# Kernel tuning notes

Hardware: AMD Instinct MI355X
Metric: run time of the kernel (lower is better)

Reference implementation:

```python
import jax, jax.numpy as jnp
import numpy as np

P_DROP = 0.6  # F.dropout default training=True in the original forward

def setup_inputs() -> dict:
    key = jax.random.key(0)
    k1, k2, k3, k4 = jax.random.split(key, 4)
    B, T, V, F, K, O = 32, 12, 1000, 64, 3, 64
    x = jax.random.normal(k1, (B, T, V, F), dtype=jnp.float32)
    Att = jax.random.uniform(k2, (V, V), dtype=jnp.float32)
    cheb = jax.random.normal(k3, (K, V, V), dtype=jnp.float32)   # Chebyshev polynomials T_k(L)
    Theta = jax.random.normal(k4, (K, F, O), dtype=jnp.float32)  # per-order feature transforms
    return {"x": x, "Att": Att, "cheb": cheb, "Theta": Theta}

def reference(x, Att, cheb, Theta):
    # x: [B,T,V,F]; Att: [V,V]; cheb: [K,V,V]; Theta: [K,F,O]
    B, T, V, F = x.shape
    K = cheb.shape[0]
    keep = 1.0 - P_DROP
    # Original draws a fresh dropout mask per (time_step, k); replicate with a fixed key.
    mask = jax.random.bernoulli(jax.random.key(42), keep, (T, K, V, V))
    TkA = cheb * Att                                   # [K,V,V] attention-weighted polynomial
    M = jnp.where(mask, TkA[None] / keep, 0.0)         # [T,K,V,V] inverted dropout
    # rhs = T_k_with_at @ graph_signal, batched over (b,t,k)
    rhs = jnp.einsum('tkuv,btvf->btkuf', M, x)         # [B,T,K,V,F]
    # sum_k rhs_k @ Theta_k  -> [B,T,V,O]; matches permute(0,3,1,2) of stacked outputs
    out = jnp.einsum('btkuf,kfo->btuo', rhs, Theta)
    return jax.nn.relu(out)
```

## Files before the change

kernel.cpp:

```cpp
#include <hip/hip_runtime.h>
#include <hip/hip_bf16.h>
#include <stdint.h>


typedef __attribute__((ext_vector_type(8))) short short8;
typedef __attribute__((ext_vector_type(4))) float f32x4;

__device__ __forceinline__ ushort f2bf(float f) {
  __hip_bfloat16 h = __float2bfloat16(f);
  return *reinterpret_cast<ushort*>(&h);
}

__device__ __forceinline__ void threefry2x32(uint32_t c0, uint32_t c1,
                                             uint32_t& o0, uint32_t& o1) {
  const uint32_t ks0 = 0u;
  const uint32_t ks1 = 42u;
  const uint32_t ks2 = ks0 ^ ks1 ^ 0x1BD11BDAu;
  uint32_t x0 = c0 + ks0;
  uint32_t x1 = c1 + ks1;
#define TFR(r) { x0 += x1; x1 = (x1 << (r)) | (x1 >> (32 - (r))); x1 ^= x0; }
  TFR(13) TFR(15) TFR(26) TFR(6)
  x0 += ks1; x1 += ks2 + 1u;
  TFR(17) TFR(29) TFR(16) TFR(24)
  x0 += ks2; x1 += ks0 + 2u;
  TFR(13) TFR(15) TFR(26) TFR(6)
  x0 += ks0; x1 += ks1 + 3u;
  TFR(17) TFR(29) TFR(16) TFR(24)
  x0 += ks1; x1 += ks2 + 4u;
  TFR(13) TFR(15) TFR(26) TFR(6)
  x0 += ks2; x1 += ks0 + 5u;
#undef TFR
  o0 = x0; o1 = x1;
}

__global__ void build_m(const float* __restrict__ Att,
                        const float* __restrict__ cheb,
                        ushort* __restrict__ Mws) {
  const uint32_t idx = blockIdx.x * 256u + threadIdx.x;
  const uint32_t vp = idx & 1023u;
  const uint32_t up = (idx >> 10) & 1023u;
  const uint32_t tk = idx >> 20;
  float val = 0.f;
  if ((vp < 1000u) & (up < 1000u)) {
    const uint32_t flat = (tk * 1000u + up) * 1000u + vp;
    uint32_t o0, o1;
    threefry2x32(0u, flat, o0, o1);
    const uint32_t bits = o0 ^ o1;
    const float u = __uint_as_float((bits >> 9) | 0x3f800000u) - 1.0f;
    if (u < 0.4f) {
      val = cheb[(tk % 3u) * 1000000u + up * 1000u + vp] *
            Att[up * 1000u + vp] * 2.5f;
    }
  }
  Mws[idx] = f2bf(val);
}

__global__ void transpose_x(const float* __restrict__ x,
                            ushort* __restrict__ xt) {
  __shared__ float lt[64][65];
  const int vc = blockIdx.x, t = blockIdx.y, b = blockIdx.z;
  const int tid = threadIdx.x;
  const int v0 = vc * 64;
#pragma unroll
  for (int i = 0; i < 4; ++i) {
    const int c = i * 256 + tid;
    const int vi = c >> 4, f4 = c & 15;
    float4 q = make_float4(0.f, 0.f, 0.f, 0.f);
    if (v0 + vi < 1000)
      q = *(const float4*)(x + ((((size_t)b * 12 + t) * 1000 + v0 + vi) << 6) + f4 * 4);
    lt[f4 * 4 + 0][vi] = q.x;
    lt[f4 * 4 + 1][vi] = q.y;
    lt[f4 * 4 + 2][vi] = q.z;
    lt[f4 * 4 + 3][vi] = q.w;
  }
  __syncthreads();
  const int f = tid >> 2, g = tid & 3;
  alignas(16) ushort tmp[16];
#pragma unroll
  for (int j = 0; j < 16; ++j) tmp[j] = f2bf(lt[f][g * 16 + j]);
  const size_t base = ((size_t)(t * 2048 + b * 64 + f)) << 10;
  *(uint4*)(xt + base + v0 + g * 16)     = *(const uint4*)&tmp[0];
  *(uint4*)(xt + base + v0 + g * 16 + 8) = *(const uint4*)&tmp[8];
}

#define LDT 72

#define MFMA(a, b, c) __builtin_amdgcn_mfma_f32_16x16x32_bf16((a), (b), (c), 0, 0, 0)

#define STAGE_LOAD(P0, P1, P2, P3, P4, P5, P6, P7, CO)                        \
  do {                                                                        \
    P0 = *(const uint4*)(Mws + ga0 + (CO));                                   \
    P1 = *(const uint4*)(Mws + ga1 + (CO));                                   \
    P2 = *(const uint4*)(Mws + ga0 + 1048576 + (CO));                         \
    P3 = *(const uint4*)(Mws + ga1 + 1048576 + (CO));                         \
    P4 = *(const uint4*)(Mws + ga0 + 2097152 + (CO));                         \
    P5 = *(const uint4*)(Mws + ga1 + 2097152 + (CO));                         \
    P6 = *(const uint4*)(xt + gx0 + (CO));                                    \
    P7 = *(const uint4*)(xt + gx1 + (CO));                                    \
  } while (0)

#define STAGE_WRITE(P0, P1, P2, P3, P4, P5, P6, P7, BP)                       \
  do {                                                                        \
    *(uint4*)&(BP)[da0]         = P0;                                         \
    *(uint4*)&(BP)[da1]         = P1;                                         \
    *(uint4*)&(BP)[8192 + da0]  = P2;                                         \
    *(uint4*)&(BP)[8192 + da1]  = P3;                                         \
    *(uint4*)&(BP)[16384 + da0] = P4;                                         \
    *(uint4*)&(BP)[16384 + da1] = P5;                                         \
    *(uint4*)&(BP)[24576 + da0] = P6;                                         \
    *(uint4*)&(BP)[24576 + da1] = P7;                                         \
  } while (0)

#define BURST(BP)                                                             \
  do {                                                                        \
    const ushort* sAc = (BP);                                                 \
    const ushort* sBc = (BP) + 24576;                                         \
    _Pragma("unroll")                                                         \
    for (int ks = 0; ks < 2; ++ks) {                                          \
      short8 bv[4];                                                           \
      _Pragma("unroll")                                                       \
      for (int ni = 0; ni < 4; ++ni) {                                        \
        const int row = wn * 64 + ni * 16 + l15;                              \
        bv[ni] = *(const short8*)&sBc[row * 64 + (((ks * 4 + quad) ^ rsw) * 8)]; \
      }                                                                       \
      _Pragma("unroll")                                                       \
      for (int k = 0; k < 3; ++k) {                                           \
        short8 av[2];                                                         \
        _Pragma("unroll")                                                     \
        for (int mi = 0; mi < 2; ++mi) {                                      \
          const int row = wu * 32 + mi * 16 + l15;                            \
          av[mi] = *(const short8*)&sAc[k * 8192 + row * 64 +                 \
                                        (((ks * 4 + quad) ^ rsw) * 8)];       \
        }                                                                     \
        _Pragma("unroll")                                                     \
        for (int mi = 0; mi < 2; ++mi)                                        \
          _Pragma("unroll")                                                   \
          for (int ni = 0; ni < 4; ++ni)                                      \
            pacc[k][mi][ni] = MFMA(av[mi], bv[ni], pacc[k][mi][ni]);          \
      }                                                                       \
    }                                                                         \
  } while (0)

#define SOFT_BARRIER()                                                        \
  do {                                                                        \
    asm volatile("s_waitcnt lgkmcnt(0)" ::: "memory");                        \
    __builtin_amdgcn_s_barrier();                                             \
    __builtin_amdgcn_sched_barrier(0);                                        \
  } while (0)

__global__ __launch_bounds__(512, 2)
void cheb_main(const ushort* __restrict__ Mws, const ushort* __restrict__ xt,
               const float* __restrict__ Theta, float* __restrict__ out) {
  __shared__ __align__(16) ushort smem[65536];
  const int tid = threadIdx.x;
  const int lane = tid & 63;
  const int w = tid >> 6;
  const int wu = w >> 1, wn = w & 1;
  const int quad = lane >> 4, l15 = lane & 15;
  const int nt = blockIdx.x, ut = blockIdx.y, t = blockIdx.z;
  const int u0 = ut * 128, n0 = nt * 128;

  ushort* buf0 = smem;
  ushort* buf1 = smem + 32768;
  ushort* sP  = smem + w * (32 * LDT);
  ushort* sTh = smem + 24576;

  const int srow = lane >> 3;
  const int gchunk = (lane & 7) ^ srow;
  const int rsw = l15 & 7;

  const size_t mbase = (size_t)(t * 3) << 20;
  const size_t xrow0 = (size_t)(t * 2048 + n0);

  const int rr0 = 8 * (w * 2 + 0) + srow;
  const int rr1 = 8 * (w * 2 + 1) + srow;
  const size_t ga0 = mbase + ((size_t)(u0 + rr0) << 10) + gchunk * 8;
  const size_t ga1 = mbase + ((size_t)(u0 + rr1) << 10) + gchunk * 8;
  const size_t gx0 = ((xrow0 + rr0) << 10) + gchunk * 8;
  const size_t gx1 = ((xrow0 + rr1) << 10) + gchunk * 8;
  const int da0 = (w * 2 + 0) * 512 + lane * 8;
  const int da1 = (w * 2 + 1) * 512 + lane * 8;

  f32x4 pacc[3][2][4];
#pragma unroll
  for (int k = 0; k < 3; ++k)
#pragma unroll
    for (int i = 0; i < 2; ++i)
#pragma unroll
      for (int j = 0; j < 4; ++j) pacc[k][i][j] = f32x4{0.f, 0.f, 0.f, 0.f};

  uint4 p0, p1, p2, p3, p4, p5, p6, p7;
  uint4 q0, q1, q2, q3, q4, q5, q6, q7;

  STAGE_LOAD(q0, q1, q2, q3, q4, q5, q6, q7, 0);
  STAGE_LOAD(p0, p1, p2, p3, p4, p5, p6, p7, 64);
  STAGE_WRITE(q0, q1, q2, q3, q4, q5, q6, q7, buf0);
  __syncthreads();

#pragma unroll 1
  for (int it = 0; it < 8; ++it) {
    const int vc = it * 2;
    if (vc < 14) STAGE_LOAD(q0, q1, q2, q3, q4, q5, q6, q7, (size_t)(vc + 2) * 64);
    __builtin_amdgcn_s_setprio(1);
    BURST(buf0);
    __builtin_amdgcn_s_setprio(0);
    if (vc < 15) STAGE_WRITE(p0, p1, p2, p3, p4, p5, p6, p7, buf1);
    SOFT_BARRIER();
    if (vc + 1 < 14) STAGE_LOAD(p0, p1, p2, p3, p4, p5, p6, p7, (size_t)(vc + 3) * 64);
    __builtin_amdgcn_s_setprio(1);
    BURST(buf1);
    __builtin_amdgcn_s_setprio(0);
    if (vc + 1 < 15) STAGE_WRITE(q0, q1, q2, q3, q4, q5, q6, q7, buf0);
    SOFT_BARRIER();
  }

  f32x4 oacc[2][4];
#pragma unroll
  for (int i = 0; i < 2; ++i)
#pragma unroll
    for (int j = 0; j < 4; ++j) oacc[i][j] = f32x4{0.f, 0.f, 0.f, 0.f};

#pragma unroll
  for (int k = 0; k < 3; ++k) {
    __syncthreads();
#pragma unroll
    for (int mi = 0; mi < 2; ++mi)
#pragma unroll
      for (int ni = 0; ni < 4; ++ni)
#pragma unroll
        for (int r = 0; r < 4; ++r)
          sP[(mi * 16 + quad * 4 + r) * LDT + ni * 16 + l15] = f2bf(pacc[k][mi][ni][r]);
    for (int e = tid; e < 4096; e += 512) {
      const int f = e >> 6, o = e & 63;
      sTh[o * LDT + f] = f2bf(Theta[k * 4096 + e]);
    }
    __syncthreads();
#pragma unroll
    for (int ks = 0; ks < 2; ++ks) {
      short8 a2[2], b2[4];
#pragma unroll
      for (int mi = 0; mi < 2; ++mi)
        a2[mi] = *(const short8*)&sP[(mi * 16 + l15) * LDT + ks * 32 + quad * 8];
#pragma unroll
      for (int ni = 0; ni < 4; ++ni)
        b2[ni] = *(const short8*)&sTh[(ni * 16 + l15) * LDT + ks * 32 + quad * 8];
#pragma unroll
      for (int mi = 0; mi < 2; ++mi)
#pragma unroll
        for (int ni = 0; ni < 4; ++ni)
          oacc[mi][ni] = MFMA(a2[mi], b2[ni], oacc[mi][ni]);
    }
  }

#pragma unroll
  for (int mi = 0; mi < 2; ++mi) {
    const int u_base = u0 + wu * 32 + mi * 16 + quad * 4;
#pragma unroll
    for (int ni = 0; ni < 4; ++ni) {
      const int n = n0 + wn * 64 + ni * 16 + l15;
      const int b = n >> 6, oo = n & 63;
      float* op = out + (((size_t)b * 12 + t) * 1000) * 64 + oo;
#pragma unroll
      for (int r = 0; r < 4; ++r) {
        const int u = u_base + r;
        if (u < 1000) op[(size_t)u * 64] = fmaxf(oacc[mi][ni][r], 0.f);
      }
    }
  }
}

extern "C" void kernel_launch(void* const* d_in, const int* in_sizes, int n_in,
                              void* d_out, int out_size, void* d_ws, size_t ws_size,
                              hipStream_t stream) {
  const float* x     = (const float*)d_in[0];
  const float* Att   = (const float*)d_in[1];
  const float* cheb  = (const float*)d_in[2];
  const float* Theta = (const float*)d_in[3];
  float* out = (float*)d_out;

  ushort* Mws = (ushort*)d_ws;
  ushort* xtw = Mws + 37748736ull;

  build_m<<<147456, 256, 0, stream>>>(Att, cheb, Mws);
  transpose_x<<<dim3(16, 12, 32), 256, 0, stream>>>(x, xtw);
  cheb_main<<<dim3(16, 8, 12), 512, 0, stream>>>(Mws, xtw, Theta, out);
}
```

Measured before the change: 295.3 us.

## Pre-swizzle M into MFMA fragment layout and load A operands directly to registers

build_m now writes the dropout-masked Chebyshev matrix in an MFMA-fragment-ordered layout, so cheb_main loads A operands straight from global memory into registers and no longer stages them through LDS. Only the x tile is double-buffered in shared memory, which shrinks the LDS footprint. The grid is flattened to 1D with ut as the fastest index, so blocks that share an x tile are adjacent. Launch bounds drop to one block per SM, and each lane now issues many uncoalesced-by-tile global loads per step, which risks exposed latency and more register pressure.

```diff
diff --git a/kernel.cpp b/kernel.cpp
--- a/kernel.cpp
+++ b/kernel.cpp
@@ -35,11 +35,16 @@
 
 __global__ void build_m(const float* __restrict__ Att,
                         const float* __restrict__ cheb,
-                        ushort* __restrict__ Mws) {
+                        ushort* __restrict__ Mf) {
   const uint32_t idx = blockIdx.x * 256u + threadIdx.x;
-  const uint32_t vp = idx & 1023u;
-  const uint32_t up = (idx >> 10) & 1023u;
+  const uint32_t j = idx & 7u;
+  const uint32_t lane = (idx >> 3) & 63u;
+  const uint32_t ks = (idx >> 9) & 1u;
+  const uint32_t c = (idx >> 10) & 15u;
+  const uint32_t u16 = (idx >> 14) & 63u;
   const uint32_t tk = idx >> 20;
+  const uint32_t up = u16 * 16u + (lane & 15u);
+  const uint32_t vp = c * 64u + ks * 32u + (lane >> 4) * 8u + j;
   float val = 0.f;
   if ((vp < 1000u) & (up < 1000u)) {
     const uint32_t flat = (tk * 1000u + up) * 1000u + vp;
@@ -52,7 +57,7 @@
             Att[up * 1000u + vp] * 2.5f;
     }
   }
-  Mws[idx] = f2bf(val);
+  Mf[idx] = f2bf(val);
 }
 
 __global__ void transpose_x(const float* __restrict__ x,
@@ -87,34 +92,9 @@
 
 #define MFMA(a, b, c) __builtin_amdgcn_mfma_f32_16x16x32_bf16((a), (b), (c), 0, 0, 0)
 
-#define STAGE_LOAD(P0, P1, P2, P3, P4, P5, P6, P7, CO)                        \
-  do {                                                                        \
-    P0 = *(const uint4*)(Mws + ga0 + (CO));                                   \
-    P1 = *(const uint4*)(Mws + ga1 + (CO));                                   \
-    P2 = *(const uint4*)(Mws + ga0 + 1048576 + (CO));                         \
-    P3 = *(const uint4*)(Mws + ga1 + 1048576 + (CO));                         \
-    P4 = *(const uint4*)(Mws + ga0 + 2097152 + (CO));                         \
-    P5 = *(const uint4*)(Mws + ga1 + 2097152 + (CO));                         \
-    P6 = *(const uint4*)(xt + gx0 + (CO));                                    \
-    P7 = *(const uint4*)(xt + gx1 + (CO));                                    \
-  } while (0)
-
-#define STAGE_WRITE(P0, P1, P2, P3, P4, P5, P6, P7, BP)                       \
-  do {                                                                        \
-    *(uint4*)&(BP)[da0]         = P0;                                         \
-    *(uint4*)&(BP)[da1]         = P1;                                         \
-    *(uint4*)&(BP)[8192 + da0]  = P2;                                         \
-    *(uint4*)&(BP)[8192 + da1]  = P3;                                         \
-    *(uint4*)&(BP)[16384 + da0] = P4;                                         \
-    *(uint4*)&(BP)[16384 + da1] = P5;                                         \
-    *(uint4*)&(BP)[24576 + da0] = P6;                                         \
-    *(uint4*)&(BP)[24576 + da1] = P7;                                         \
-  } while (0)
-
 #define BURST(BP)                                                             \
   do {                                                                        \
-    const ushort* sAc = (BP);                                                 \
-    const ushort* sBc = (BP) + 24576;                                         \
+    const ushort* sBc = (BP);                                                 \
     _Pragma("unroll")                                                         \
     for (int ks = 0; ks < 2; ++ks) {                                          \
       short8 bv[4];                                                           \
@@ -124,21 +104,25 @@
         bv[ni] = *(const short8*)&sBc[row * 64 + (((ks * 4 + quad) ^ rsw) * 8)]; \
       }                                                                       \
       _Pragma("unroll")                                                       \
-      for (int k = 0; k < 3; ++k) {                                           \
-        short8 av[2];                                                         \
-        _Pragma("unroll")                                                     \
-        for (int mi = 0; mi < 2; ++mi) {                                      \
-          const int row = wu * 32 + mi * 16 + l15;                            \
-          av[mi] = *(const short8*)&sAc[k * 8192 + row * 64 +                 \
-                                        (((ks * 4 + quad) ^ rsw) * 8)];       \
-        }                                                                     \
+      for (int k = 0; k < 3; ++k)                                             \
         _Pragma("unroll")                                                     \
         for (int mi = 0; mi < 2; ++mi)                                        \
           _Pragma("unroll")                                                   \
           for (int ni = 0; ni < 4; ++ni)                                      \
-            pacc[k][mi][ni] = MFMA(av[mi], bv[ni], pacc[k][mi][ni]);          \
-      }                                                                       \
+            pacc[k][mi][ni] = MFMA(afr[k][mi][ks], bv[ni], pacc[k][mi][ni]);  \
     }                                                                         \
+  } while (0)
+
+#define LOAD_A(VC)                                                            \
+  do {                                                                        \
+    _Pragma("unroll")                                                         \
+    for (int k = 0; k < 3; ++k)                                               \
+      _Pragma("unroll")                                                       \
+      for (int mi = 0; mi < 2; ++mi)                                          \
+        _Pragma("unroll")                                                     \
+        for (int ks = 0; ks < 2; ++ks)                                        \
+          afr[k][mi][ks] = *(const short8*)(Mf + fb[k][mi] +                  \
+                             (size_t)(VC) * 1024 + ks * 512 + lane * 8);      \
   } while (0)
 
 #define SOFT_BARRIER()                                                        \
@@ -148,39 +132,45 @@
     __builtin_amdgcn_sched_barrier(0);                                        \
   } while (0)
 
-__global__ __launch_bounds__(512, 2)
-void cheb_main(const ushort* __restrict__ Mws, const ushort* __restrict__ xt,
+__global__ __launch_bounds__(512, 1)
+void cheb_main(const ushort* __restrict__ Mf, const ushort* __restrict__ xt,
                const float* __restrict__ Theta, float* __restrict__ out) {
-  __shared__ __align__(16) ushort smem[65536];
+  __shared__ __align__(16) ushort smem[23040];
   const int tid = threadIdx.x;
   const int lane = tid & 63;
   const int w = tid >> 6;
   const int wu = w >> 1, wn = w & 1;
   const int quad = lane >> 4, l15 = lane & 15;
-  const int nt = blockIdx.x, ut = blockIdx.y, t = blockIdx.z;
+  const int bid = blockIdx.x;
+  const int nt = (bid >> 3) & 15;
+  const int ut = bid & 7;
+  const int t  = bid >> 7;
   const int u0 = ut * 128, n0 = nt * 128;
 
   ushort* buf0 = smem;
-  ushort* buf1 = smem + 32768;
+  ushort* buf1 = smem + 8192;
   ushort* sP  = smem + w * (32 * LDT);
-  ushort* sTh = smem + 24576;
+  ushort* sTh = smem + 18432;
 
   const int srow = lane >> 3;
   const int gchunk = (lane & 7) ^ srow;
   const int rsw = l15 & 7;
 
-  const size_t mbase = (size_t)(t * 3) << 20;
   const size_t xrow0 = (size_t)(t * 2048 + n0);
-
   const int rr0 = 8 * (w * 2 + 0) + srow;
   const int rr1 = 8 * (w * 2 + 1) + srow;
-  const size_t ga0 = mbase + ((size_t)(u0 + rr0) << 10) + gchunk * 8;
-  const size_t ga1 = mbase + ((size_t)(u0 + rr1) << 10) + gchunk * 8;
   const size_t gx0 = ((xrow0 + rr0) << 10) + gchunk * 8;
   const size_t gx1 = ((xrow0 + rr1) << 10) + gchunk * 8;
   const int da0 = (w * 2 + 0) * 512 + lane * 8;
   const int da1 = (w * 2 + 1) * 512 + lane * 8;
 
+  size_t fb[3][2];
+#pragma unroll
+  for (int k = 0; k < 3; ++k)
+#pragma unroll
+    for (int mi = 0; mi < 2; ++mi)
+      fb[k][mi] = ((size_t)((t * 3 + k) * 64 + ut * 8 + wu * 2 + mi)) << 14;
+
   f32x4 pacc[3][2][4];
 #pragma unroll
   for (int k = 0; k < 3; ++k)
@@ -189,28 +179,39 @@
 #pragma unroll
       for (int j = 0; j < 4; ++j) pacc[k][i][j] = f32x4{0.f, 0.f, 0.f, 0.f};
 
-  uint4 p0, p1, p2, p3, p4, p5, p6, p7;
-  uint4 q0, q1, q2, q3, q4, q5, q6, q7;
-
-  STAGE_LOAD(q0, q1, q2, q3, q4, q5, q6, q7, 0);
-  STAGE_LOAD(p0, p1, p2, p3, p4, p5, p6, p7, 64);
-  STAGE_WRITE(q0, q1, q2, q3, q4, q5, q6, q7, buf0);
+  short8 afr[3][2][2];
+  uint4 p0, p1;
+
+  p0 = *(const uint4*)(xt + gx0);
+  p1 = *(const uint4*)(xt + gx1);
+  *(uint4*)&buf0[da0] = p0;
+  *(uint4*)&buf0[da1] = p1;
   __syncthreads();
 
 #pragma unroll 1
   for (int it = 0; it < 8; ++it) {
     const int vc = it * 2;
-    if (vc < 14) STAGE_LOAD(q0, q1, q2, q3, q4, q5, q6, q7, (size_t)(vc + 2) * 64);
+    LOAD_A(vc);
+    p0 = *(const uint4*)(xt + gx0 + (size_t)(vc + 1) * 64);
+    p1 = *(const uint4*)(xt + gx1 + (size_t)(vc + 1) * 64);
     __builtin_amdgcn_s_setprio(1);
     BURST(buf0);
     __builtin_amdgcn_s_setprio(0);
-    if (vc < 15) STAGE_WRITE(p0, p1, p2, p3, p4, p5, p6, p7, buf1);
+    *(uint4*)&buf1[da0] = p0;
+    *(uint4*)&buf1[da1] = p1;
     SOFT_BARRIER();
-    if (vc + 1 < 14) STAGE_LOAD(p0, p1, p2, p3, p4, p5, p6, p7, (size_t)(vc + 3) * 64);
+    LOAD_A(vc + 1);
+    if (vc + 1 < 15) {
+      p0 = *(const uint4*)(xt + gx0 + (size_t)(vc + 2) * 64);
+      p1 = *(const uint4*)(xt + gx1 + (size_t)(vc + 2) * 64);
+    }
     __builtin_amdgcn_s_setprio(1);
     BURST(buf1);
     __builtin_amdgcn_s_setprio(0);
-    if (vc + 1 < 15) STAGE_WRITE(q0, q1, q2, q3, q4, q5, q6, q7, buf0);
+    if (vc + 1 < 15) {
+      *(uint4*)&buf0[da0] = p0;
+      *(uint4*)&buf0[da1] = p1;
+    }
     SOFT_BARRIER();
   }
 
@@ -278,10 +279,10 @@
   const float* Theta = (const float*)d_in[3];
   float* out = (float*)d_out;
 
-  ushort* Mws = (ushort*)d_ws;
-  ushort* xtw = Mws + 37748736ull;
-
-  build_m<<<147456, 256, 0, stream>>>(Att, cheb, Mws);
+  ushort* Mf  = (ushort*)d_ws;
+  ushort* xtw = Mf + 37748736ull;
+
+  build_m<<<147456, 256, 0, stream>>>(Att, cheb, Mf);
   transpose_x<<<dim3(16, 12, 32), 256, 0, stream>>>(x, xtw);
-  cheb_main<<<dim3(16, 8, 12), 512, 0, stream>>>(Mws, xtw, Theta, out);
-}
+  cheb_main<<<1536, 512, 0, stream>>>(Mf, xtw, Theta, out);
+}
```

Result: slower. 306.1 us (+3.7%).
